# Performance work log

Hardware: AMD Instinct MI355X
Metric: run time of the kernel (lower is better)

The kernel has to match this reference:

```python
import jax, jax.numpy as jnp
import numpy as np

UNITS = 2048
INPUT_DIM = 2048
BATCH = 8192


def setup_inputs() -> dict:
    key = jax.random.key(0)
    k_x, k_w = jax.random.split(key)
    inputs = jax.random.normal(k_x, (BATCH, INPUT_DIM), dtype=jnp.float32)
    # random_normal initializer in keras defaults to stddev=0.05
    w = jax.random.normal(k_w, (INPUT_DIM, UNITS), dtype=jnp.float32) * 0.05
    b = jnp.zeros((UNITS,), dtype=jnp.float32)
    return {"inputs": inputs, "w": w, "b": b}


def reference(inputs, w, b):
    # matmul + bias
    result = jnp.matmul(inputs, w) + b  # [B, units]
    # per-row: if first element > 0.5, add 1 to whole row, else subtract 1
    cond = result[:, :1] > 0.5  # [B, 1], broadcasts over row
    return jnp.where(cond, result + 1.0, result - 1.0)
```

## Files before the change

kernel.cpp:

```cpp
#include <hip/hip_runtime.h>
#include <hip/hip_bf16.h>
#include <stdint.h>

#define M_DIM 8192
#define N_DIM 2048
#define K_DIM 2048

typedef __attribute__((ext_vector_type(8))) short bf16x8;
typedef __attribute__((ext_vector_type(8))) short short8;
typedef __attribute__((ext_vector_type(4))) float f32x4;
typedef __attribute__((ext_vector_type(16))) float f32x16;

static __device__ __forceinline__ unsigned short f2bf(float f) {
  union { float f; unsigned u; } a; a.f = f;
  unsigned u = a.u;
  u += 0x7FFFu + ((u >> 16) & 1u);
  return (unsigned short)(u >> 16);
}

static __device__ __forceinline__ void async16(void* lds, const void* g) {
  __builtin_amdgcn_global_load_lds(
      (const __attribute__((address_space(1))) unsigned int*)g,
      (__attribute__((address_space(3))) unsigned int*)lds, 16, 0, 0);
}

#define BAR()                                \
  do {                                       \
    asm volatile("" ::: "memory");           \
    __builtin_amdgcn_s_barrier();            \
    asm volatile("" ::: "memory");           \
  } while (0)
#define VMCNT(n) asm volatile("s_waitcnt vmcnt(" #n ")" ::: "memory")

__global__ __launch_bounds__(256) void k_transW(const float* __restrict__ W,
                                                unsigned short* __restrict__ Wt,
                                                float* __restrict__ wcol) {
  __shared__ float tile[64][65];
  const int bx = blockIdx.x & 31;
  const int by = blockIdx.x >> 5;
  const int n0 = bx * 64, k0 = by * 64;
  const int t = threadIdx.x;
  #pragma unroll
  for (int i = 0; i < 16; ++i) {
    int lin = i * 256 + t;
    int r = lin >> 6, c = lin & 63;
    float v = W[(size_t)(k0 + r) * N_DIM + n0 + c];
    tile[r][c] = v;
    if (bx == 0 && c == 0) wcol[k0 + r] = v;
  }
  __syncthreads();
  #pragma unroll
  for (int i = 0; i < 16; ++i) {
    int lin = i * 256 + t;
    int r = lin >> 6, c = lin & 63;
    Wt[(size_t)(n0 + r) * K_DIM + k0 + c] = f2bf(tile[c][r]);
  }
}

__global__ __launch_bounds__(256) void k_convX(const float* __restrict__ X,
    const float* __restrict__ wcol, const float* __restrict__ b,
    unsigned short* __restrict__ Xb, float* __restrict__ adj) {
  const int m = blockIdx.x;
  const int t = threadIdx.x;
  const float4* xr = (const float4*)(X + (size_t)m * K_DIM);
  const float4* wc = (const float4*)wcol;
  float4 x0 = xr[2 * t], x1 = xr[2 * t + 1];
  float4 w0 = wc[2 * t], w1 = wc[2 * t + 1];
  short8 o;
  o[0] = (short)f2bf(x0.x); o[1] = (short)f2bf(x0.y);
  o[2] = (short)f2bf(x0.z); o[3] = (short)f2bf(x0.w);
  o[4] = (short)f2bf(x1.x); o[5] = (short)f2bf(x1.y);
  o[6] = (short)f2bf(x1.z); o[7] = (short)f2bf(x1.w);
  *(short8*)(Xb + (size_t)m * K_DIM + t * 8) = o;
  double s = (double)x0.x * w0.x + (double)x0.y * w0.y +
             (double)x0.z * w0.z + (double)x0.w * w0.w +
             (double)x1.x * w1.x + (double)x1.y * w1.y +
             (double)x1.z * w1.z + (double)x1.w * w1.w;
  #pragma unroll
  for (int off = 32; off > 0; off >>= 1) s += __shfl_down(s, off, 64);
  __shared__ double red[4];
  if ((t & 63) == 0) red[t >> 6] = s;
  __syncthreads();
  if (t == 0) {
    double tot = red[0] + red[1] + red[2] + red[3] + (double)b[0];
    adj[m] = (tot > 0.5) ? 1.0f : -1.0f;
  }
}

__device__ __forceinline__ void stage_unit(char* ldsc,
    const unsigned short* __restrict__ src, int row0, int kt,
    int isB, int sel, int wid, int l) {
  char* base = ldsc + (size_t)(kt & 1) * 65536 + (size_t)isB * 32768;
  const int p = ((l >> 2) & 15) + 16 * (l & 1) + 32 * (((l >> 1) ^ (l >> 5)) & 1);
  #pragma unroll
  for (int j = 0; j < 2; ++j) {
    int idx = wid * 2 + j;
    int q = idx >> 2, sc = idx & 3;
    int sr = isB ? (q * 2 + sel) : ((q & 1) + sel * 2 + (q >> 1) * 4);
    int grow = row0 + sr * 32 + (p & 31);
    int gcol = kt * 64 + sc * 16 + (p >> 5) * 8;
    async16(base + (size_t)(sr * 4 + sc) * 1024,
            src + (size_t)grow * K_DIM + gcol);
  }
}

__global__ __launch_bounds__(512, 1) void k_gemm8(
    const unsigned short* __restrict__ A,
    const unsigned short* __restrict__ B,
    const float* __restrict__ bias,
    const float* __restrict__ adj,
    float* __restrict__ out) {
  __shared__ unsigned short lds[2 * 2 * 256 * 64];
  char* ldsc = (char*)lds;

  const int t = threadIdx.x;
  const int wid = t >> 6, l = t & 63;
  const int wm = wid >> 2, wn = wid & 3;

  const int bid = blockIdx.x;
  const int swz = (bid & 7) * 32 + (bid >> 3);
  const int bm = swz >> 3, bn = swz & 7;
  const int m0 = bm * 256, n0 = bn * 256;

  const int rloc = l & 15, qloc = l >> 4;
  const int rdoff = (rloc * 64 + qloc * 16) ^ ((rloc & 8) << 2);

  f32x16 acc[4][2] = {};

#define STG(isB, sel, kt) \
  stage_unit(ldsc, (isB) ? B : A, (isB) ? n0 : m0, kt, isB, sel, wid, l)

#define RD_A(MH)                                                            \
  _Pragma("unroll") for (int mb2 = 0; mb2 < 2; ++mb2) {                     \
    const char* abase = ab +                                                \
        (size_t)((wm * 4 + (MH) * 2 + mb2) * 4) * 1024 + rdoff;             \
    _Pragma("unroll") for (int ks = 0; ks < 4; ++ks)                        \
      af[mb2][ks] = *(const bf16x8*)(abase + ks * 1024);                    \
  }

#define RD_B(DST, NH)                                                       \
  {                                                                         \
    const char* bbase = bb +                                                \
        (size_t)((wn * 2 + (NH)) * 4) * 1024 + rdoff;                       \
    _Pragma("unroll") for (int ks = 0; ks < 4; ++ks)                        \
      DST[ks] = *(const bf16x8*)(bbase + ks * 1024);                        \
  }

#define PHASE(BUF, MH, NH, READ_STMT, STAGE_STMT, WAIT_STMT)                \
  {                                                                         \
    const char* ab = ldsc + (size_t)(BUF) * 65536;                          \
    const char* bb = ab + 32768;                                            \
    (void)ab; (void)bb;                                                     \
    READ_STMT;                                                              \
    STAGE_STMT;                                                             \
    BAR();                                                                  \
    __builtin_amdgcn_s_setprio(1);                                          \
    _Pragma("unroll") for (int ks = 0; ks < 4; ++ks)                        \
      _Pragma("unroll") for (int mb2 = 0; mb2 < 2; ++mb2) {                 \
        acc[(MH) * 2 + mb2][NH] = __builtin_amdgcn_mfma_f32_32x32x16_bf16(  \
            af[mb2][ks], ((NH) ? bv1 : bv0)[ks], acc[(MH) * 2 + mb2][NH],   \
            0, 0, 0);                                                       \
      }                                                                     \
    __builtin_amdgcn_s_setprio(0);                                          \
    WAIT_STMT;                                                              \
    BAR();                                                                  \
  }

  STG(0, 0, 0); STG(1, 0, 0); STG(1, 1, 0); STG(0, 1, 0);
  VMCNT(2);
  BAR();

  for (int j = 0; j < 31; ++j) {
    const int buf = j & 1;
    const int nt = j + 1;
    bf16x8 af[2][4], bv0[4], bv1[4];
    PHASE(buf, 0, 0, RD_A(0); RD_B(bv0, 0); RD_B(bv1, 1),
          STG(0, 0, nt), );
    PHASE(buf, 0, 1, , STG(1, 0, nt), VMCNT(4));
    PHASE(buf, 1, 0, RD_A(1), STG(1, 1, nt), );
    PHASE(buf, 1, 1, , STG(0, 1, nt), VMCNT(2));
  }
  {
    bf16x8 af[2][4], bv0[4], bv1[4];
    PHASE(1, 0, 0, RD_A(0); RD_B(bv0, 0); RD_B(bv1, 1), , );
    PHASE(1, 0, 1, , , VMCNT(0));
    PHASE(1, 1, 0, RD_A(1), , );
    PHASE(1, 1, 1, , , );
  }

#undef PHASE
#undef RD_A
#undef RD_B
#undef STG

  #pragma unroll
  for (int mb = 0; mb < 4; ++mb) {
    #pragma unroll
    for (int nb = 0; nb < 2; ++nb) {
      const int col = n0 + wn * 64 + nb * 32 + (l & 31);
      const float bvs = bias[col];
      #pragma unroll
      for (int rg = 0; rg < 4; ++rg) {
        const int rowb = m0 + wm * 128 + mb * 32 + rg * 8 + 4 * (l >> 5);
        const float4 adjv = *(const float4*)&adj[rowb];
        #pragma unroll
        for (int rr = 0; rr < 4; ++rr)
          out[(size_t)(rowb + rr) * N_DIM + col] =
              acc[mb][nb][rg * 4 + rr] + bvs + adjv[rr];
      }
    }
  }
}

__global__ __launch_bounds__(256) void k_gemm_f32(const float* __restrict__ X,
    const float* __restrict__ W, const float* __restrict__ b,
    float* __restrict__ out) {
  __shared__ float As[16][16];
  __shared__ float Bs[16][17];
  const int bn = blockIdx.x & 127, bm = blockIdx.x >> 7;
  const int tx = threadIdx.x & 15, ty = threadIdx.x >> 4;
  const int row = bm * 16 + ty, col = bn * 16 + tx;
  float acc = 0.f;
  for (int k0 = 0; k0 < K_DIM; k0 += 16) {
    As[ty][tx] = X[(size_t)row * K_DIM + k0 + tx];
    Bs[ty][tx] = W[(size_t)(k0 + ty) * N_DIM + col];
    __syncthreads();
    #pragma unroll
    for (int kk = 0; kk < 16; ++kk) acc += As[ty][kk] * Bs[kk][tx];
    __syncthreads();
  }
  out[(size_t)row * N_DIM + col] = acc + b[col];
}

__global__ __launch_bounds__(256) void k_rowadj(float* __restrict__ out) {
  const int m = blockIdx.x;
  const float c0 = out[(size_t)m * N_DIM];
  __syncthreads();
  const float a = (c0 > 0.5f) ? 1.0f : -1.0f;
  for (int n = threadIdx.x; n < N_DIM; n += 256)
    out[(size_t)m * N_DIM + n] += a;
}

extern "C" void kernel_launch(void* const* d_in, const int* in_sizes, int n_in,
                              void* d_out, int out_size, void* d_ws, size_t ws_size,
                              hipStream_t stream) {
  const float* X = (const float*)d_in[0];
  const float* W = (const float*)d_in[1];
  const float* b = (const float*)d_in[2];
  float* out = (float*)d_out;

  const size_t XB_OFF   = 0;
  const size_t WT_OFF   = (size_t)M_DIM * K_DIM * 2;
  const size_t ADJ_OFF  = WT_OFF + (size_t)N_DIM * K_DIM * 2;
  const size_t WCOL_OFF = ADJ_OFF + (size_t)M_DIM * 4;
  const size_t NEED     = WCOL_OFF + (size_t)K_DIM * 4;

  if (ws_size >= NEED) {
    unsigned short* Xb  = (unsigned short*)((char*)d_ws + XB_OFF);
    unsigned short* Wt  = (unsigned short*)((char*)d_ws + WT_OFF);
    float* adj  = (float*)((char*)d_ws + ADJ_OFF);
    float* wcol = (float*)((char*)d_ws + WCOL_OFF);
    k_transW<<<dim3(1024), dim3(256), 0, stream>>>(W, Wt, wcol);
    k_convX<<<dim3(M_DIM), dim3(256), 0, stream>>>(X, wcol, b, Xb, adj);
    k_gemm8<<<dim3((M_DIM / 256) * (N_DIM / 256)), dim3(512), 0, stream>>>(
        Xb, Wt, b, adj, out);
  } else {
    k_gemm_f32<<<dim3((M_DIM / 16) * (N_DIM / 16)), dim3(256), 0, stream>>>(
        X, W, b, out);
    k_rowadj<<<dim3(M_DIM), dim3(256), 0, stream>>>(out);
  }
}
```

Measured before the change: 99.10 us.

## Restructure GEMM main loop into three-barrier software pipeline with register prefetch

Replaces the four-phase per-iteration schedule, which had two barriers per phase, with a three-stage schedule that prefetches the next tile's A/B fragments into registers before the final MFMA cluster. Staging of the next k-tile starts one step earlier, and the barrier count per k-step drops from eight to three. The aim is to overlap LDS reads and global-to-LDS copies with MFMA work and cut synchronization stalls. The cost is more live fragment registers (af0/af1) and a more delicate vmcnt/barrier ordering against buffer reuse.

```diff
diff --git a/kernel.cpp b/kernel.cpp
--- a/kernel.cpp
+++ b/kernel.cpp
@@ -130,65 +130,92 @@
 #define STG(isB, sel, kt) \
   stage_unit(ldsc, (isB) ? B : A, (isB) ? n0 : m0, kt, isB, sel, wid, l)
 
-#define RD_A(MH)                                                            \
+#define RD_A(DST, MH, ABUF)                                                 \
   _Pragma("unroll") for (int mb2 = 0; mb2 < 2; ++mb2) {                     \
-    const char* abase = ab +                                                \
+    const char* abase = (ABUF) +                                            \
         (size_t)((wm * 4 + (MH) * 2 + mb2) * 4) * 1024 + rdoff;             \
     _Pragma("unroll") for (int ks = 0; ks < 4; ++ks)                        \
-      af[mb2][ks] = *(const bf16x8*)(abase + ks * 1024);                    \
-  }
-
-#define RD_B(DST, NH)                                                       \
+      DST[mb2][ks] = *(const bf16x8*)(abase + ks * 1024);                   \
+  }
+
+#define RD_B(DST, NH, BBUF)                                                 \
   {                                                                         \
-    const char* bbase = bb +                                                \
+    const char* bbase = (BBUF) +                                            \
         (size_t)((wn * 2 + (NH)) * 4) * 1024 + rdoff;                       \
     _Pragma("unroll") for (int ks = 0; ks < 4; ++ks)                        \
       DST[ks] = *(const bf16x8*)(bbase + ks * 1024);                        \
   }
 
-#define PHASE(BUF, MH, NH, READ_STMT, STAGE_STMT, WAIT_STMT)                \
-  {                                                                         \
-    const char* ab = ldsc + (size_t)(BUF) * 65536;                          \
-    const char* bb = ab + 32768;                                            \
-    (void)ab; (void)bb;                                                     \
-    READ_STMT;                                                              \
-    STAGE_STMT;                                                             \
-    BAR();                                                                  \
-    __builtin_amdgcn_s_setprio(1);                                          \
-    _Pragma("unroll") for (int ks = 0; ks < 4; ++ks)                        \
-      _Pragma("unroll") for (int mb2 = 0; mb2 < 2; ++mb2) {                 \
-        acc[(MH) * 2 + mb2][NH] = __builtin_amdgcn_mfma_f32_32x32x16_bf16(  \
-            af[mb2][ks], ((NH) ? bv1 : bv0)[ks], acc[(MH) * 2 + mb2][NH],   \
-            0, 0, 0);                                                       \
-      }                                                                     \
-    __builtin_amdgcn_s_setprio(0);                                          \
-    WAIT_STMT;                                                              \
-    BAR();                                                                  \
-  }
+#define MFMA_CL(MH, NH, AF, BV)                                             \
+  __builtin_amdgcn_s_setprio(1);                                            \
+  _Pragma("unroll") for (int ks = 0; ks < 4; ++ks)                          \
+    _Pragma("unroll") for (int mb2 = 0; mb2 < 2; ++mb2)                     \
+      acc[(MH) * 2 + mb2][NH] = __builtin_amdgcn_mfma_f32_32x32x16_bf16(    \
+          AF[mb2][ks], BV[ks], acc[(MH) * 2 + mb2][NH], 0, 0, 0);           \
+  __builtin_amdgcn_s_setprio(0);
+
+  bf16x8 af0[2][4], af1[2][4], bv0[4], bv1[4];
 
   STG(0, 0, 0); STG(1, 0, 0); STG(1, 1, 0); STG(0, 1, 0);
-  VMCNT(2);
+  STG(0, 0, 1);
+  VMCNT(4);
   BAR();
-
-  for (int j = 0; j < 31; ++j) {
-    const int buf = j & 1;
+  RD_A(af0, 0, ldsc);
+  RD_B(bv0, 0, ldsc + 32768);
+
+  for (int j = 0; j < 30; ++j) {
+    const char* ab  = ldsc + (size_t)(j & 1) * 65536;
+    const char* bb  = ab + 32768;
+    const char* abn = ldsc + (size_t)((j + 1) & 1) * 65536;
+    const char* bbn = abn + 32768;
     const int nt = j + 1;
-    bf16x8 af[2][4], bv0[4], bv1[4];
-    PHASE(buf, 0, 0, RD_A(0); RD_B(bv0, 0); RD_B(bv1, 1),
-          STG(0, 0, nt), );
-    PHASE(buf, 0, 1, , STG(1, 0, nt), VMCNT(4));
-    PHASE(buf, 1, 0, RD_A(1), STG(1, 1, nt), );
-    PHASE(buf, 1, 1, , STG(0, 1, nt), VMCNT(2));
+    RD_B(bv1, 1, bb);
+    STG(1, 0, nt);
+    MFMA_CL(0, 0, af0, bv0);
+    VMCNT(4); BAR();
+    RD_A(af1, 1, ab);
+    STG(1, 1, nt); STG(0, 1, nt);
+    MFMA_CL(0, 1, af0, bv1);
+    MFMA_CL(1, 0, af1, bv0);
+    VMCNT(4); BAR();
+    RD_A(af0, 0, abn);
+    RD_B(bv0, 0, bbn);
+    STG(0, 0, nt + 1);
+    MFMA_CL(1, 1, af1, bv1);
+    VMCNT(4); BAR();
   }
   {
-    bf16x8 af[2][4], bv0[4], bv1[4];
-    PHASE(1, 0, 0, RD_A(0); RD_B(bv0, 0); RD_B(bv1, 1), , );
-    PHASE(1, 0, 1, , , VMCNT(0));
-    PHASE(1, 1, 0, RD_A(1), , );
-    PHASE(1, 1, 1, , , );
-  }
-
-#undef PHASE
+    const char* ab  = ldsc;
+    const char* bb  = ab + 32768;
+    const char* abn = ldsc + 65536;
+    const char* bbn = abn + 32768;
+    RD_B(bv1, 1, bb);
+    STG(1, 0, 31);
+    MFMA_CL(0, 0, af0, bv0);
+    VMCNT(4); BAR();
+    RD_A(af1, 1, ab);
+    STG(1, 1, 31); STG(0, 1, 31);
+    MFMA_CL(0, 1, af0, bv1);
+    MFMA_CL(1, 0, af1, bv0);
+    VMCNT(4); BAR();
+    RD_A(af0, 0, abn);
+    RD_B(bv0, 0, bbn);
+    MFMA_CL(1, 1, af1, bv1);
+    VMCNT(2); BAR();
+  }
+  {
+    const char* ab = ldsc + 65536;
+    const char* bb = ab + 32768;
+    RD_B(bv1, 1, bb);
+    MFMA_CL(0, 0, af0, bv0);
+    VMCNT(0); BAR();
+    RD_A(af1, 1, ab);
+    MFMA_CL(0, 1, af0, bv1);
+    MFMA_CL(1, 0, af1, bv0);
+    MFMA_CL(1, 1, af1, bv1);
+  }
+
+#undef MFMA_CL
 #undef RD_A
 #undef RD_B
 #undef STG
```

Result: no change. 99.50 us (+0.4%).
